# Kernel optimization log

Measured on AMD Instinct MI355X. Metric: run time of the kernel, lower is better.

## Reference

```python
import jax, jax.numpy as jnp
import numpy as np

NUM_SRC = 200000
NUM_DST = 100000
NUM_EDGES = 1600000
IN_DIM = 128
HID = 256
OUT_DIM = 128


def layer_norm(h, g, b, eps=1e-5):
    mu = jnp.mean(h, axis=-1, keepdims=True)
    var = jnp.mean((h - mu) ** 2, axis=-1, keepdims=True)
    return (h - mu) * jax.lax.rsqrt(var + eps) * g + b


def setup_inputs() -> dict:
    key = jax.random.key(0)
    ks = jax.random.split(key, 8)
    s_in = 1.0 / np.sqrt(IN_DIM)
    s_hid = 1.0 / np.sqrt(HID)
    return {
        "x": jax.random.normal(ks[0], (NUM_SRC, IN_DIM), dtype=jnp.float32),
        "w_l": jax.random.normal(ks[1], (IN_DIM, HID), dtype=jnp.float32) * s_in,
        "b_l": jnp.zeros((HID,), dtype=jnp.float32),
        "w_r": jax.random.normal(ks[2], (IN_DIM, HID), dtype=jnp.float32) * s_in,
        "ln1_g": jnp.ones((HID,), dtype=jnp.float32),
        "ln1_b": jnp.zeros((HID,), dtype=jnp.float32),
        "w_out": jax.random.normal(ks[3], (HID, OUT_DIM), dtype=jnp.float32) * s_hid,
        "b_out": jnp.zeros((OUT_DIM,), dtype=jnp.float32),
        "ln2_g": jnp.ones((OUT_DIM,), dtype=jnp.float32),
        "ln2_b": jnp.zeros((OUT_DIM,), dtype=jnp.float32),
        "edge_src": jax.random.randint(ks[4], (NUM_EDGES,), 0, NUM_SRC, dtype=jnp.int64),
        "edge_dst": jax.random.randint(ks[5], (NUM_EDGES,), 0, NUM_DST, dtype=jnp.int64),
    }


def reference(x, w_l, b_l, w_r, ln1_g, ln1_b, w_out, b_out, ln2_g, ln2_b, edge_src, edge_dst):
    # SAGEConv bipartite: targets are the first NUM_DST rows of x
    x_tgt = x[:NUM_DST]
    # mean aggregation of source-node messages at destination nodes
    msgs = x[edge_src]  # [E, IN_DIM] irregular gather
    summed = jax.ops.segment_sum(msgs, edge_dst, num_segments=NUM_DST)
    cnt = jax.ops.segment_sum(jnp.ones((NUM_EDGES,), dtype=x.dtype), edge_dst, num_segments=NUM_DST)
    mean_nbr = summed / jnp.maximum(cnt, 1.0)[:, None]
    # out = lin_l(aggr) + lin_r(x_target); dropout p=0 is identity
    h = mean_nbr @ w_l + b_l + x_tgt @ w_r
    h = layer_norm(h, ln1_g, ln1_b)
    h = jax.nn.gelu(h, approximate=False)
    out = h @ w_out + b_out
    out = layer_norm(out, ln2_g, ln2_b)
    return out
```

## Files before the change

### kernel.cpp

```cpp
#include <hip/hip_runtime.h>
#include <math.h>

#define NSRC 200000
#define NDST 100000
#define NEDGE 1600000

typedef unsigned int uint32;
typedef unsigned short u16;

typedef short short8 __attribute__((ext_vector_type(8)));
typedef float f32x4 __attribute__((ext_vector_type(4)));

__device__ __forceinline__ u16 f2b(float f) {
  uint32 u = __float_as_uint(f);
  u += 0x7fffu + ((u >> 16) & 1u);
  return (u16)(u >> 16);
}
__device__ __forceinline__ float b2f_lo(uint32 u) { return __uint_as_float(u << 16); }
__device__ __forceinline__ float b2f_hi(uint32 u) { return __uint_as_float(u & 0xffff0000u); }

#define BCHUNK 2048
#define NB_BUCKET ((NEDGE + BCHUNK - 1) / BCHUNK)
#define NB_W 384
#define NB_CVT 25000

__global__ __launch_bounds__(256) void k_prep(const float* __restrict__ x, u16* __restrict__ xb,
                                              const float* __restrict__ wl,
                                              const float* __restrict__ wr,
                                              const float* __restrict__ wo,
                                              u16* __restrict__ wp1f, u16* __restrict__ wp2f,
                                              const int do_cvt, const int* __restrict__ src,
                                              const int* __restrict__ dst, int* __restrict__ cnt,
                                              int* __restrict__ csr, const int cap) {
  __shared__ int sd[BCHUNK], ss[BCHUNK];
  if (blockIdx.x < NB_BUCKET) {
    int base = blockIdx.x * BCHUNK;
    for (int i = threadIdx.x; i < BCHUNK; i += 256) {
      int e = base + i;
      sd[i] = (e < NEDGE) ? dst[e] : -1;
      ss[i] = (e < NEDGE) ? src[e] : 0;
    }
    __syncthreads();
    for (int p = 0; p < 8; p++) {
      int lo = p * 12500;
      int hi = lo + 12500;
      for (int i = threadIdx.x; i < BCHUNK; i += 256) {
        int d = sd[i];
        if (d >= lo && d < hi) {
          int pos = atomicAdd(&cnt[d], 1);
          if (pos < cap) csr[(size_t)d * cap + pos] = ss[i];
        }
      }
    }
    return;
  }
  int bid = blockIdx.x - NB_BUCKET;
  if (bid < NB_W) {
    int t = bid * 256 + threadIdx.x;
    if (t < 65536) {
      int j = t & 7, lane = (t >> 3) & 63, nt = (t >> 9) & 3, kc = (t >> 11) & 7, w = t >> 14;
      int k = kc * 32 + (lane >> 4) * 8 + j;
      int n = w * 64 + nt * 16 + (lane & 15);
      float v = (k < 128) ? wl[k * 256 + n] : wr[(k - 128) * 256 + n];
      wp1f[t] = f2b(v);
    } else {
      int t2 = t - 65536;
      int j = t2 & 7, lane = (t2 >> 3) & 63, nt = (t2 >> 9) & 1, kc = (t2 >> 10) & 7, w = t2 >> 13;
      int k = kc * 32 + (lane >> 4) * 8 + j;
      int n = w * 32 + nt * 16 + (lane & 15);
      wp2f[t2] = f2b(wo[k * 128 + n]);
    }
    return;
  }
  if (!do_cvt) return;
  int idx = (bid - NB_W) * 256 + threadIdx.x;
  size_t i = (size_t)idx * 4;
  if (i < (size_t)NSRC * 128) {
    float4 f = *(const float4*)(x + i);
    uint2 o;
    o.x = (uint32)f2b(f.x) | ((uint32)f2b(f.y) << 16);
    o.y = (uint32)f2b(f.z) | ((uint32)f2b(f.w) << 16);
    *(uint2*)(xb + i) = o;
  }
}

#define LDAH 264

__global__ __launch_bounds__(256) void k_fused(
    const u16* __restrict__ xb, const float* __restrict__ xf, const int x_is_bf16,
    const int* __restrict__ csr, const int* __restrict__ cnt, const int cap,
    const u16* __restrict__ wp1f, const u16* __restrict__ wp2f,
    const float* __restrict__ bl_g, const float* __restrict__ g1_g, const float* __restrict__ b1_g,
    const float* __restrict__ bo_g, const float* __restrict__ g2_g, const float* __restrict__ b2_g,
    float* __restrict__ out) {
  __shared__ __align__(16) u16 AH_lds[64 * LDAH];
  __shared__ float2 stats[4][64];
  __shared__ float2 stats2[64];

  const int tid = threadIdx.x;
  const int wave = tid >> 6;
  const int lane = tid & 63;
  const int l15 = lane & 15;
  const int q = lane >> 4;
  const int row0 = blockIdx.x * 64;

  {
    const int sub = tid & 15;
    const int dgrp = tid >> 4;
#pragma unroll 1
    for (int pass = 0; pass < 4; pass++) {
      int r = pass * 16 + dgrp;
      int d = row0 + r;
      u16* rowp = AH_lds + r * LDAH;
      if (d < NDST) {
        int n = cnt[d];
        int m = n < cap ? n : cap;
        const int* cp = csr + (size_t)d * cap;
        float a[8] = {0, 0, 0, 0, 0, 0, 0, 0};
        if (x_is_bf16) {
          int i = 0;
          for (; i + 3 < m; i += 4) {
            int s0 = cp[i];
            int s1 = cp[i + 1];
            int s2 = cp[i + 2];
            int s3 = cp[i + 3];
            uint4 p0 = *(const uint4*)(xb + (size_t)s0 * 128 + sub * 8);
            uint4 p1 = *(const uint4*)(xb + (size_t)s1 * 128 + sub * 8);
            uint4 p2 = *(const uint4*)(xb + (size_t)s2 * 128 + sub * 8);
            uint4 p3 = *(const uint4*)(xb + (size_t)s3 * 128 + sub * 8);
            a[0] += b2f_lo(p0.x); a[1] += b2f_hi(p0.x);
            a[2] += b2f_lo(p0.y); a[3] += b2f_hi(p0.y);
            a[4] += b2f_lo(p0.z); a[5] += b2f_hi(p0.z);
            a[6] += b2f_lo(p0.w); a[7] += b2f_hi(p0.w);
            a[0] += b2f_lo(p1.x); a[1] += b2f_hi(p1.x);
            a[2] += b2f_lo(p1.y); a[3] += b2f_hi(p1.y);
            a[4] += b2f_lo(p1.z); a[5] += b2f_hi(p1.z);
            a[6] += b2f_lo(p1.w); a[7] += b2f_hi(p1.w);
            a[0] += b2f_lo(p2.x); a[1] += b2f_hi(p2.x);
            a[2] += b2f_lo(p2.y); a[3] += b2f_hi(p2.y);
            a[4] += b2f_lo(p2.z); a[5] += b2f_hi(p2.z);
            a[6] += b2f_lo(p2.w); a[7] += b2f_hi(p2.w);
            a[0] += b2f_lo(p3.x); a[1] += b2f_hi(p3.x);
            a[2] += b2f_lo(p3.y); a[3] += b2f_hi(p3.y);
            a[4] += b2f_lo(p3.z); a[5] += b2f_hi(p3.z);
            a[6] += b2f_lo(p3.w); a[7] += b2f_hi(p3.w);
          }
          for (; i < m; i++) {
            int s0 = cp[i];
            uint4 p = *(const uint4*)(xb + (size_t)s0 * 128 + sub * 8);
            a[0] += b2f_lo(p.x); a[1] += b2f_hi(p.x);
            a[2] += b2f_lo(p.y); a[3] += b2f_hi(p.y);
            a[4] += b2f_lo(p.z); a[5] += b2f_hi(p.z);
            a[6] += b2f_lo(p.w); a[7] += b2f_hi(p.w);
          }
        } else {
          for (int i = 0; i < m; i++) {
            int s = cp[i];
            const float* p = xf + (size_t)s * 128 + sub * 8;
            float4 f0 = *(const float4*)p;
            float4 f1 = *(const float4*)(p + 4);
            a[0] += f0.x; a[1] += f0.y; a[2] += f0.z; a[3] += f0.w;
            a[4] += f1.x; a[5] += f1.y; a[6] += f1.z; a[7] += f1.w;
          }
        }
        float sc = 1.f / (float)(n > 0 ? n : 1);
        uint4 o;
        o.x = (uint32)f2b(a[0] * sc) | ((uint32)f2b(a[1] * sc) << 16);
        o.y = (uint32)f2b(a[2] * sc) | ((uint32)f2b(a[3] * sc) << 16);
        o.z = (uint32)f2b(a[4] * sc) | ((uint32)f2b(a[5] * sc) << 16);
        o.w = (uint32)f2b(a[6] * sc) | ((uint32)f2b(a[7] * sc) << 16);
        *(uint4*)(rowp + sub * 8) = o;
        uint4 xv;
        if (x_is_bf16) {
          xv = *(const uint4*)(xb + (size_t)d * 128 + sub * 8);
        } else {
          const float* p = xf + (size_t)d * 128 + sub * 8;
          float4 f0 = *(const float4*)p;
          float4 f1 = *(const float4*)(p + 4);
          xv.x = (uint32)f2b(f0.x) | ((uint32)f2b(f0.y) << 16);
          xv.y = (uint32)f2b(f0.z) | ((uint32)f2b(f0.w) << 16);
          xv.z = (uint32)f2b(f1.x) | ((uint32)f2b(f1.y) << 16);
          xv.w = (uint32)f2b(f1.z) | ((uint32)f2b(f1.w) << 16);
        }
        *(uint4*)(rowp + 128 + sub * 8) = xv;
      } else {
        uint4 z = {0u, 0u, 0u, 0u};
        *(uint4*)(rowp + sub * 8) = z;
        *(uint4*)(rowp + 128 + sub * 8) = z;
      }
    }
  }
  __syncthreads();

  f32x4 acc[4][4];
#pragma unroll
  for (int i = 0; i < 4; i++)
#pragma unroll
    for (int j = 0; j < 4; j++) acc[i][j] = (f32x4){0.f, 0.f, 0.f, 0.f};

#pragma unroll 2
  for (int kc = 0; kc < 8; kc++) {
    short8 bfr[4];
    const uint4* bsrc = (const uint4*)(wp1f + (((size_t)wave * 8 + kc) * 4) * 512);
#pragma unroll
    for (int nt = 0; nt < 4; nt++) bfr[nt] = ((const short8*)(bsrc + nt * 64))[lane];
    short8 af[4];
#pragma unroll
    for (int mt = 0; mt < 4; mt++)
      af[mt] = *(const short8*)(AH_lds + (16 * mt + l15) * LDAH + kc * 32 + q * 8);
#pragma unroll
    for (int mt = 0; mt < 4; mt++)
#pragma unroll
      for (int nt = 0; nt < 4; nt++)
        acc[mt][nt] = __builtin_amdgcn_mfma_f32_16x16x32_bf16(af[mt], bfr[nt], acc[mt][nt], 0, 0, 0);
  }

  float bl[4], g1[4], b1[4];
#pragma unroll
  for (int nt = 0; nt < 4; nt++) {
    int c = 64 * wave + 16 * nt + l15;
    bl[nt] = bl_g[c]; g1[nt] = g1_g[c]; b1[nt] = b1_g[c];
  }
#pragma unroll
  for (int mt = 0; mt < 4; mt++)
#pragma unroll
    for (int nt = 0; nt < 4; nt++)
#pragma unroll
      for (int r = 0; r < 4; r++) acc[mt][nt][r] += bl[nt];

#pragma unroll
  for (int mt = 0; mt < 4; mt++)
#pragma unroll
    for (int r = 0; r < 4; r++) {
      float s = 0.f, s2 = 0.f;
#pragma unroll
      for (int nt = 0; nt < 4; nt++) { float v = acc[mt][nt][r]; s += v; s2 += v * v; }
#pragma unroll
      for (int m = 1; m < 16; m <<= 1) { s += __shfl_xor(s, m, 64); s2 += __shfl_xor(s2, m, 64); }
      if (l15 == 0) stats[wave][16 * mt + 4 * q + r] = make_float2(s, s2);
    }
  __syncthreads();
  if (tid < 64) {
    float S = 0.f, Q = 0.f;
#pragma unroll
    for (int w = 0; w < 4; w++) { float2 t = stats[w][tid]; S += t.x; Q += t.y; }
    float mu = S * (1.f / 256.f);
    float var = Q * (1.f / 256.f) - mu * mu;
    stats2[tid] = make_float2(mu, rsqrtf(var + 1e-5f));
  }
  __syncthreads();
#pragma unroll
  for (int mt = 0; mt < 4; mt++)
#pragma unroll
    for (int r = 0; r < 4; r++) {
      int row = 16 * mt + 4 * q + r;
      float2 st = stats2[row];
#pragma unroll
      for (int nt = 0; nt < 4; nt++) {
        float v = acc[mt][nt][r];
        float hn = (v - st.x) * st.y * g1[nt] + b1[nt];
        float t2 = hn * hn;
        float u = fmaf(0.044715f * t2, hn, hn);
        float ge = hn / (1.f + __expf(-1.5957691216f * u));
        AH_lds[row * LDAH + 64 * wave + 16 * nt + l15] = f2b(ge);
      }
    }
  __syncthreads();

  f32x4 acc2[4][2];
#pragma unroll
  for (int i = 0; i < 4; i++)
#pragma unroll
    for (int j = 0; j < 2; j++) acc2[i][j] = (f32x4){0.f, 0.f, 0.f, 0.f};

#pragma unroll 2
  for (int kc = 0; kc < 8; kc++) {
    short8 bfr[2];
    const uint4* bsrc = (const uint4*)(wp2f + (((size_t)wave * 8 + kc) * 2) * 512);
#pragma unroll
    for (int nt = 0; nt < 2; nt++) bfr[nt] = ((const short8*)(bsrc + nt * 64))[lane];
    short8 af[4];
#pragma unroll
    for (int mt = 0; mt < 4; mt++)
      af[mt] = *(const short8*)(AH_lds + (16 * mt + l15) * LDAH + kc * 32 + q * 8);
#pragma unroll
    for (int mt = 0; mt < 4; mt++)
#pragma unroll
      for (int nt = 0; nt < 2; nt++)
        acc2[mt][nt] = __builtin_amdgcn_mfma_f32_16x16x32_bf16(af[mt], bfr[nt], acc2[mt][nt], 0, 0, 0);
  }

  float bo[2], g2[2], b2c[2];
#pragma unroll
  for (int nt = 0; nt < 2; nt++) {
    int c = 32 * wave + 16 * nt + l15;
    bo[nt] = bo_g[c]; g2[nt] = g2_g[c]; b2c[nt] = b2_g[c];
  }
#pragma unroll
  for (int mt = 0; mt < 4; mt++)
#pragma unroll
    for (int nt = 0; nt < 2; nt++)
#pragma unroll
      for (int r = 0; r < 4; r++) acc2[mt][nt][r] += bo[nt];

#pragma unroll
  for (int mt = 0; mt < 4; mt++)
#pragma unroll
    for (int r = 0; r < 4; r++) {
      float s = 0.f, s2 = 0.f;
#pragma unroll
      for (int nt = 0; nt < 2; nt++) { float v = acc2[mt][nt][r]; s += v; s2 += v * v; }
#pragma unroll
      for (int m = 1; m < 16; m <<= 1) { s += __shfl_xor(s, m, 64); s2 += __shfl_xor(s2, m, 64); }
      if (l15 == 0) stats[wave][16 * mt + 4 * q + r] = make_float2(s, s2);
    }
  __syncthreads();
  if (tid < 64) {
    float S = 0.f, Q = 0.f;
#pragma unroll
    for (int w = 0; w < 4; w++) { float2 t = stats[w][tid]; S += t.x; Q += t.y; }
    float mu = S * (1.f / 128.f);
    float var = Q * (1.f / 128.f) - mu * mu;
    stats2[tid] = make_float2(mu, rsqrtf(var + 1e-5f));
  }
  __syncthreads();
#pragma unroll
  for (int mt = 0; mt < 4; mt++)
#pragma unroll
    for (int r = 0; r < 4; r++) {
      int row = 16 * mt + 4 * q + r;
      int R = row0 + row;
      if (R < NDST) {
        float2 st = stats2[row];
#pragma unroll
        for (int nt = 0; nt < 2; nt++) {
          float v = acc2[mt][nt][r];
          out[(size_t)R * 128 + 32 * wave + 16 * nt + l15] = (v - st.x) * st.y * g2[nt] + b2c[nt];
        }
      }
    }
}

extern "C" void kernel_launch(void* const* d_in, const int* in_sizes, int n_in,
                              void* d_out, int out_size, void* d_ws, size_t ws_size,
                              hipStream_t stream) {
  const float* x   = (const float*)d_in[0];
  const float* w_l = (const float*)d_in[1];
  const float* b_l = (const float*)d_in[2];
  const float* w_r = (const float*)d_in[3];
  const float* g1  = (const float*)d_in[4];
  const float* b1  = (const float*)d_in[5];
  const float* w_o = (const float*)d_in[6];
  const float* b_o = (const float*)d_in[7];
  const float* g2  = (const float*)d_in[8];
  const float* b2  = (const float*)d_in[9];
  const int* esrc  = (const int*)d_in[10];
  const int* edst  = (const int*)d_in[11];
  float* out = (float*)d_out;

  char* ws = (char*)d_ws;
  size_t off = 0;
  auto alloc = [&](size_t bytes) -> void* {
    off = (off + 255) & ~(size_t)255;
    void* p = ws + off;
    off += bytes;
    return p;
  };
  int* cnt   = (int*)alloc((size_t)NDST * 4);
  u16* wp1f  = (u16*)alloc((size_t)65536 * 2);
  u16* wp2f  = (u16*)alloc((size_t)32768 * 2);

  size_t rem = (ws_size > off + 512) ? (ws_size - off - 512) : 0;
  size_t xb_bytes = (size_t)NSRC * 128 * 2;
  int cap;
  int x_is_bf16;
  if (rem >= (size_t)NDST * 64 * 4 + xb_bytes) { cap = 64; x_is_bf16 = 1; }
  else if (rem >= (size_t)NDST * 64 * 4)       { cap = 64; x_is_bf16 = 0; }
  else if (rem >= (size_t)NDST * 32 * 4)       { cap = 32; x_is_bf16 = 0; }
  else                                         { cap = 16; x_is_bf16 = 0; }
  int* csr = (int*)alloc((size_t)NDST * cap * 4);
  u16* xb = x_is_bf16 ? (u16*)alloc(xb_bytes) : nullptr;

  hipMemsetAsync(cnt, 0, (size_t)NDST * 4, stream);
  k_prep<<<NB_BUCKET + NB_W + NB_CVT, 256, 0, stream>>>(x, xb, w_l, w_r, w_o, wp1f, wp2f,
                                                        x_is_bf16, esrc, edst, cnt, csr, cap);
  k_fused<<<(NDST + 63) / 64, 256, 0, stream>>>(xb, x, x_is_bf16, csr, cnt, cap, wp1f, wp2f,
                                                b_l, g1, b1, b_o, g2, b2, out);
}
```

Measured before the change: 415.8 us.

## Replace per-destination CSR atomics with 64-row bucket binning and LDS-local CSR

The per-destination global atomic CSR build (100k counters, padded rows of 64 slots) is replaced. The new build does a two-level bucketing: 128 blocks histogram edges into 1563 buckets of 64 destinations using shared-memory atomics, reserve slots with one global atomic per bucket, then scatter packed (src<<6|dst_lo) pairs. The fused kernel then builds each block's per-row neighbor lists in LDS from its bucket before gathering. This cuts global atomic traffic and CSR memory, but adds LDS use in the fused kernel (which may lower occupancy) and caps buckets at 1344 edges and rows at 64 neighbors. Overflow beyond those caps is silently dropped, and packing the source index into 26 bits relies on NSRC fitting.

```diff
diff --git a/kernel.cpp b/kernel.cpp
--- a/kernel.cpp
+++ b/kernel.cpp
@@ -19,8 +19,10 @@
 __device__ __forceinline__ float b2f_lo(uint32 u) { return __uint_as_float(u << 16); }
 __device__ __forceinline__ float b2f_hi(uint32 u) { return __uint_as_float(u & 0xffff0000u); }
 
-#define BCHUNK 2048
-#define NB_BUCKET ((NEDGE + BCHUNK - 1) / BCHUNK)
+#define NBKT 1563
+#define BKTCAP 1344
+#define NB_H 128
+#define EPH (NEDGE / NB_H)
 #define NB_W 384
 #define NB_CVT 25000
 
@@ -30,31 +32,34 @@
                                               const float* __restrict__ wo,
                                               u16* __restrict__ wp1f, u16* __restrict__ wp2f,
                                               const int do_cvt, const int* __restrict__ src,
-                                              const int* __restrict__ dst, int* __restrict__ cnt,
-                                              int* __restrict__ csr, const int cap) {
-  __shared__ int sd[BCHUNK], ss[BCHUNK];
-  if (blockIdx.x < NB_BUCKET) {
-    int base = blockIdx.x * BCHUNK;
-    for (int i = threadIdx.x; i < BCHUNK; i += 256) {
-      int e = base + i;
-      sd[i] = (e < NEDGE) ? dst[e] : -1;
-      ss[i] = (e < NEDGE) ? src[e] : 0;
-    }
+                                              const int* __restrict__ dst,
+                                              int* __restrict__ bktcnt,
+                                              int* __restrict__ pairs) {
+  __shared__ int hist[NBKT];
+  __shared__ int loff[NBKT];
+  if (blockIdx.x < NB_H) {
+    int base = blockIdx.x * EPH;
+    for (int i = threadIdx.x; i < NBKT; i += 256) hist[i] = 0;
     __syncthreads();
-    for (int p = 0; p < 8; p++) {
-      int lo = p * 12500;
-      int hi = lo + 12500;
-      for (int i = threadIdx.x; i < BCHUNK; i += 256) {
-        int d = sd[i];
-        if (d >= lo && d < hi) {
-          int pos = atomicAdd(&cnt[d], 1);
-          if (pos < cap) csr[(size_t)d * cap + pos] = ss[i];
-        }
-      }
+    for (int i = threadIdx.x; i < EPH; i += 256) atomicAdd(&hist[dst[base + i] >> 6], 1);
+    __syncthreads();
+    for (int i = threadIdx.x; i < NBKT; i += 256) {
+      int h = hist[i];
+      loff[i] = h ? atomicAdd(&bktcnt[i * 16], h) : 0;
+      hist[i] = 0;
+    }
+    __syncthreads();
+    for (int i = threadIdx.x; i < EPH; i += 256) {
+      int d = dst[base + i];
+      int s = src[base + i];
+      int bin = d >> 6;
+      int r = atomicAdd(&hist[bin], 1);
+      int pos = loff[bin] + r;
+      if (pos < BKTCAP) pairs[(size_t)bin * BKTCAP + pos] = (s << 6) | (d & 63);
     }
     return;
   }
-  int bid = blockIdx.x - NB_BUCKET;
+  int bid = blockIdx.x - NB_H;
   if (bid < NB_W) {
     int t = bid * 256 + threadIdx.x;
     if (t < 65536) {
@@ -85,10 +90,11 @@
 }
 
 #define LDAH 264
+#define LCSR_LD 65
 
 __global__ __launch_bounds__(256) void k_fused(
     const u16* __restrict__ xb, const float* __restrict__ xf, const int x_is_bf16,
-    const int* __restrict__ csr, const int* __restrict__ cnt, const int cap,
+    const int* __restrict__ pairs, const int* __restrict__ bktcnt,
     const u16* __restrict__ wp1f, const u16* __restrict__ wp2f,
     const float* __restrict__ bl_g, const float* __restrict__ g1_g, const float* __restrict__ b1_g,
     const float* __restrict__ bo_g, const float* __restrict__ g2_g, const float* __restrict__ b2_g,
@@ -96,6 +102,8 @@
   __shared__ __align__(16) u16 AH_lds[64 * LDAH];
   __shared__ float2 stats[4][64];
   __shared__ float2 stats2[64];
+  __shared__ int lcnt[64];
+  __shared__ int lcsr[64 * LCSR_LD];
 
   const int tid = threadIdx.x;
   const int wave = tid >> 6;
@@ -103,6 +111,21 @@
   const int l15 = lane & 15;
   const int q = lane >> 4;
   const int row0 = blockIdx.x * 64;
+
+  {
+    const int bkt = blockIdx.x;
+    int total = bktcnt[(size_t)bkt * 16];
+    int mp = total < BKTCAP ? total : BKTCAP;
+    if (tid < 64) lcnt[tid] = 0;
+    __syncthreads();
+    for (int i = tid; i < mp; i += 256) {
+      int v = pairs[(size_t)bkt * BKTCAP + i];
+      int d6 = v & 63;
+      int p = atomicAdd(&lcnt[d6], 1);
+      if (p < 64) lcsr[d6 * LCSR_LD + p] = v >> 6;
+    }
+    __syncthreads();
+  }
 
   {
     const int sub = tid & 15;
@@ -113,9 +136,9 @@
       int d = row0 + r;
       u16* rowp = AH_lds + r * LDAH;
       if (d < NDST) {
-        int n = cnt[d];
-        int m = n < cap ? n : cap;
-        const int* cp = csr + (size_t)d * cap;
+        int n = lcnt[r];
+        int m = n < 64 ? n : 64;
+        const int* cp = lcsr + r * LCSR_LD;
         float a[8] = {0, 0, 0, 0, 0, 0, 0, 0};
         if (x_is_bf16) {
           int i = 0;
@@ -366,24 +389,19 @@
     off += bytes;
     return p;
   };
-  int* cnt   = (int*)alloc((size_t)NDST * 4);
-  u16* wp1f  = (u16*)alloc((size_t)65536 * 2);
-  u16* wp2f  = (u16*)alloc((size_t)32768 * 2);
+  int* bktcnt = (int*)alloc((size_t)NBKT * 16 * 4);
+  u16* wp1f   = (u16*)alloc((size_t)65536 * 2);
+  u16* wp2f   = (u16*)alloc((size_t)32768 * 2);
+  int* pairs  = (int*)alloc((size_t)NBKT * BKTCAP * 4);
 
   size_t rem = (ws_size > off + 512) ? (ws_size - off - 512) : 0;
   size_t xb_bytes = (size_t)NSRC * 128 * 2;
-  int cap;
-  int x_is_bf16;
-  if (rem >= (size_t)NDST * 64 * 4 + xb_bytes) { cap = 64; x_is_bf16 = 1; }
-  else if (rem >= (size_t)NDST * 64 * 4)       { cap = 64; x_is_bf16 = 0; }
-  else if (rem >= (size_t)NDST * 32 * 4)       { cap = 32; x_is_bf16 = 0; }
-  else                                         { cap = 16; x_is_bf16 = 0; }
-  int* csr = (int*)alloc((size_t)NDST * cap * 4);
+  int x_is_bf16 = (rem >= xb_bytes) ? 1 : 0;
   u16* xb = x_is_bf16 ? (u16*)alloc(xb_bytes) : nullptr;
 
-  hipMemsetAsync(cnt, 0, (size_t)NDST * 4, stream);
-  k_prep<<<NB_BUCKET + NB_W + NB_CVT, 256, 0, stream>>>(x, xb, w_l, w_r, w_o, wp1f, wp2f,
-                                                        x_is_bf16, esrc, edst, cnt, csr, cap);
-  k_fused<<<(NDST + 63) / 64, 256, 0, stream>>>(xb, x, x_is_bf16, csr, cnt, cap, wp1f, wp2f,
-                                                b_l, g1, b1, b_o, g2, b2, out);
+  hipMemsetAsync(bktcnt, 0, (size_t)NBKT * 16 * 4, stream);
+  k_prep<<<NB_H + NB_W + NB_CVT, 256, 0, stream>>>(x, xb, w_l, w_r, w_o, wp1f, wp2f,
+                                                   x_is_bf16, esrc, edst, bktcnt, pairs);
+  k_fused<<<NBKT, 256, 0, stream>>>(xb, x, x_is_bf16, pairs, bktcnt, wp1f, wp2f,
+                                    b_l, g1, b1, b_o, g2, b2, out);
 }
```

After: 398.6 us. 1.04x faster.
